# Performance work log

Hardware: AMD Instinct MI355X
Metric: run time of the kernel (lower is better)

## Reference

```python
import jax, jax.numpy as jnp
import numpy as np

N_STEPS = 3000
DT = 0.02


def make_phi_t(n=N_STEPS, dt=DT):
    # Central-difference first-derivative operator with one-sided 2nd-order ends.
    P = np.zeros((n, n), dtype=np.float32)
    P[0, 0:3] = [-1.5, 2.0, -0.5]
    idx = np.arange(1, n - 1)
    P[idx, idx - 1] = -0.5
    P[idx, idx + 1] = 0.5
    P[n - 1, n - 3:] = [0.5, -2.0, 1.5]
    return jnp.asarray(P / dt)


def lstm_layer(x, w_ih, w_hh, b_ih, b_hh):
    # x: [B, T, I]; PyTorch gate order i, f, g, o along the 4H axis.
    B, T, _ = x.shape
    H = w_hh.shape[1]
    x_proj = jnp.einsum('bti,gi->btg', x, w_ih) + b_ih + b_hh  # [B, T, 4H]

    def step(carry, xt):
        h, c = carry
        gates = xt + h @ w_hh.T  # [B, 4H]
        i, f, g, o = jnp.split(gates, 4, axis=-1)
        c = jax.nn.sigmoid(f) * c + jax.nn.sigmoid(i) * jnp.tanh(g)
        h = jax.nn.sigmoid(o) * jnp.tanh(c)
        return (h, c), h

    h0 = jnp.zeros((B, H), x.dtype)
    (_, _), hs = jax.lax.scan(step, (h0, h0), x_proj.transpose(1, 0, 2))
    return hs.transpose(1, 0, 2)  # [B, T, H]


def setup_inputs() -> dict:
    key = jax.random.key(0)
    B, T, I, H = 64, N_STEPS, 8, 128
    ks = jax.random.split(key, 16)
    s = lambda k, shape, fan: (jax.random.normal(k, shape, jnp.float32) / np.sqrt(fan)).astype(jnp.float32)
    return {
        'x': jax.random.normal(ks[0], (B, T, I), jnp.float32),
        'w_ih0': s(ks[1], (4 * H, I), I), 'w_hh0': s(ks[2], (4 * H, H), H),
        'b_ih0': s(ks[3], (4 * H,), H), 'b_hh0': s(ks[4], (4 * H,), H),
        'w_ih1': s(ks[5], (4 * H, H), H), 'w_hh1': s(ks[6], (4 * H, H), H),
        'b_ih1': s(ks[7], (4 * H,), H), 'b_hh1': s(ks[8], (4 * H,), H),
        'fc1_w': s(ks[9], (16, H), H), 'fc1_b': s(ks[10], (16,), H),
        'fc2_w': s(ks[11], (4, 16), 16), 'fc2_b': s(ks[12], (4,), 16),
        'fc3_w': s(ks[13], (1, 4), 4), 'fc3_b': s(ks[14], (1,), 4),
    }


def reference(x, w_ih0, w_hh0, b_ih0, b_hh0, w_ih1, w_hh1, b_ih1, b_hh1,
              fc1_w, fc1_b, fc2_w, fc2_b, fc3_w, fc3_b):
    phi = make_phi_t()  # fixed [3000, 3000] FD operator (buffer, not learned)
    h = lstm_layer(x, w_ih0, w_hh0, b_ih0, b_hh0)
    h = lstm_layer(h, w_ih1, w_hh1, b_ih1, b_hh1)
    h = jax.nn.relu(h @ fc1_w.T + fc1_b)
    h = jax.nn.relu(h @ fc2_w.T + fc2_b)
    y = h @ fc3_w.T + fc3_b            # [B, T, 1]
    yt = y[:, :, 0].T                  # [T, B]
    x_tt = phi @ (phi @ yt)            # double derivative via dense matmuls
    return x_tt.T[:, :, None]          # [B, T, 1]
```

## Files before the change

### kernel.cpp

```cpp
#include <hip/hip_runtime.h>
#include <math.h>


#define T_STEPS 3000
#define BATCH   64
#define HID     128
#define GATES   512
#define CHUNK   24
#define INV_DT  50.0f

__device__ __forceinline__ float sigmoid_(float x) {
    return 1.0f / (1.0f + __expf(-x));
}
__device__ __forceinline__ float tanh_(float x) {
    return 1.0f - 2.0f / (__expf(2.0f * x) + 1.0f);
}

__global__ __launch_bounds__(512, 2)
void lstm_layer0(const float* __restrict__ x,
                 const float* __restrict__ w_ih,
                 const float* __restrict__ w_hh,
                 const float* __restrict__ b_ih,
                 const float* __restrict__ b_hh,
                 float* __restrict__ h_out)
{
    const int b = blockIdx.x;
    const int g = threadIdx.x;
    const int j = g & (HID - 1);

    __shared__ __align__(16) float h_s[HID];
    __shared__ float part_f[HID], part_g[HID], part_o[HID];

    float w[HID];
#pragma unroll
    for (int i = 0; i < HID; i += 4) {
        float4 v = *(const float4*)(w_hh + (size_t)g * HID + i);
        w[i] = v.x; w[i+1] = v.y; w[i+2] = v.z; w[i+3] = v.w;
    }
    float wi[8];
#pragma unroll
    for (int i = 0; i < 8; i += 4) {
        float4 v = *(const float4*)(w_ih + (size_t)g * 8 + i);
        wi[i] = v.x; wi[i+1] = v.y; wi[i+2] = v.z; wi[i+3] = v.w;
    }
    const float bias = b_ih[g] + b_hh[g];
    float c = 0.0f;

    if (g < HID) h_s[g] = 0.0f;
    __syncthreads();

    const float* xrow = x + (size_t)b * T_STEPS * 8;
    float* hb = h_out + (size_t)b * T_STEPS * HID;

    for (int t = 0; t < T_STEPS; ++t) {
        float4 xa = *(const float4*)(xrow + t * 8);
        float4 xc = *(const float4*)(xrow + t * 8 + 4);
        float acc = bias
                  + wi[0]*xa.x + wi[1]*xa.y + wi[2]*xa.z + wi[3]*xa.w
                  + wi[4]*xc.x + wi[5]*xc.y + wi[6]*xc.z + wi[7]*xc.w;
#pragma unroll
        for (int k4 = 0; k4 < HID / 4; ++k4) {
            float4 h4 = *(const float4*)(&h_s[4 * k4]);
            acc += w[4*k4]*h4.x + w[4*k4+1]*h4.y + w[4*k4+2]*h4.z + w[4*k4+3]*h4.w;
        }

        float sig_i = 0.0f;
        if      (g < 128) sig_i    = sigmoid_(acc);
        else if (g < 256) part_f[j] = sigmoid_(acc);
        else if (g < 384) part_g[j] = tanh_(acc);
        else              part_o[j] = sigmoid_(acc);
        __syncthreads();

        if (g < 128) {
            c = part_f[j] * c + sig_i * part_g[j];
            float h = part_o[j] * tanh_(c);
            h_s[j] = h;
            hb[(size_t)t * HID + j] = h;
        }
        __syncthreads();
    }
}

__global__ __launch_bounds__(512, 2)
void lstm_layer1(const float* __restrict__ w_ih,
                 const float* __restrict__ w_hh,
                 const float* __restrict__ b_ih,
                 const float* __restrict__ b_hh,
                 float* __restrict__ h_buf)
{
    const int b = blockIdx.x;
    const int g = threadIdx.x;
    const int j = g & (HID - 1);

    __shared__ __align__(16) float xp[CHUNK][GATES];
    __shared__ __align__(16) float h_s[HID];
    __shared__ float part_f[HID], part_g[HID], part_o[HID];

    const float bias = b_ih[g] + b_hh[g];
    float c = 0.0f;
    if (g < HID) h_s[g] = 0.0f;

    float* hb = h_buf + (size_t)b * T_STEPS * HID;
    float w[HID];
    __syncthreads();

    for (int t0 = 0; t0 < T_STEPS; t0 += CHUNK) {
#pragma unroll
        for (int i = 0; i < HID; i += 4) {
            float4 v = *(const float4*)(w_ih + (size_t)g * HID + i);
            w[i] = v.x; w[i+1] = v.y; w[i+2] = v.z; w[i+3] = v.w;
        }
        for (int tg = 0; tg < CHUNK; tg += 8) {
            float a[8];
#pragma unroll
            for (int i = 0; i < 8; ++i) a[i] = bias;
            const float* hp = hb + (size_t)(t0 + tg) * HID;
#pragma unroll
            for (int k4 = 0; k4 < HID / 4; ++k4) {
#pragma unroll
                for (int i = 0; i < 8; ++i) {
                    float4 h4 = *(const float4*)(hp + i * HID + 4 * k4);
                    a[i] += w[4*k4]*h4.x + w[4*k4+1]*h4.y
                          + w[4*k4+2]*h4.z + w[4*k4+3]*h4.w;
                }
            }
#pragma unroll
            for (int i = 0; i < 8; ++i) xp[tg + i][g] = a[i];
        }
#pragma unroll
        for (int i = 0; i < HID; i += 4) {
            float4 v = *(const float4*)(w_hh + (size_t)g * HID + i);
            w[i] = v.x; w[i+1] = v.y; w[i+2] = v.z; w[i+3] = v.w;
        }
        __syncthreads();

        for (int tt = 0; tt < CHUNK; ++tt) {
            float acc = xp[tt][g];
#pragma unroll
            for (int k4 = 0; k4 < HID / 4; ++k4) {
                float4 h4 = *(const float4*)(&h_s[4 * k4]);
                acc += w[4*k4]*h4.x + w[4*k4+1]*h4.y + w[4*k4+2]*h4.z + w[4*k4+3]*h4.w;
            }
            float sig_i = 0.0f;
            if      (g < 128) sig_i    = sigmoid_(acc);
            else if (g < 256) part_f[j] = sigmoid_(acc);
            else if (g < 384) part_g[j] = tanh_(acc);
            else              part_o[j] = sigmoid_(acc);
            __syncthreads();
            if (g < 128) {
                c = part_f[j] * c + sig_i * part_g[j];
                float h = part_o[j] * tanh_(c);
                h_s[j] = h;
                hb[(size_t)(t0 + tt) * HID + j] = h;
            }
            __syncthreads();
        }
    }
}

__global__ void fc_head(const float* __restrict__ h_buf,
                        const float* __restrict__ fc1_w, const float* __restrict__ fc1_b,
                        const float* __restrict__ fc2_w, const float* __restrict__ fc2_b,
                        const float* __restrict__ fc3_w, const float* __restrict__ fc3_b,
                        float* __restrict__ y_t)
{
    int idx = blockIdx.x * blockDim.x + threadIdx.x;
    if (idx >= T_STEPS * BATCH) return;
    int t = idx >> 6, b = idx & 63;

    const float* h = h_buf + (size_t)b * T_STEPS * HID + (size_t)t * HID;
    float hv[HID];
#pragma unroll
    for (int k = 0; k < HID; k += 4) {
        float4 v = *(const float4*)(h + k);
        hv[k] = v.x; hv[k+1] = v.y; hv[k+2] = v.z; hv[k+3] = v.w;
    }
    float y1[16];
#pragma unroll
    for (int jo = 0; jo < 16; ++jo) {
        float a = fc1_b[jo];
#pragma unroll
        for (int k = 0; k < HID; k += 4) {
            float4 wv = *(const float4*)(fc1_w + jo * HID + k);
            a += wv.x*hv[k] + wv.y*hv[k+1] + wv.z*hv[k+2] + wv.w*hv[k+3];
        }
        y1[jo] = fmaxf(a, 0.0f);
    }
    float y2[4];
#pragma unroll
    for (int jo = 0; jo < 4; ++jo) {
        float a = fc2_b[jo];
#pragma unroll
        for (int k = 0; k < 16; ++k) a += fc2_w[jo * 16 + k] * y1[k];
        y2[jo] = fmaxf(a, 0.0f);
    }
    float y = fc3_b[0];
#pragma unroll
    for (int k = 0; k < 4; ++k) y += fc3_w[k] * y2[k];

    y_t[idx] = y;
}

__global__ void deriv_k(const float* __restrict__ in,
                        float* __restrict__ outp,
                        int transpose_out)
{
    int idx = blockIdx.x * blockDim.x + threadIdx.x;
    if (idx >= T_STEPS * BATCH) return;
    int t = idx >> 6, b = idx & 63;
    float v;
    if (t == 0) {
        v = (-1.5f * in[b] + 2.0f * in[64 + b] - 0.5f * in[128 + b]) * INV_DT;
    } else if (t == T_STEPS - 1) {
        v = (0.5f * in[(t-2)*64 + b] - 2.0f * in[(t-1)*64 + b] + 1.5f * in[t*64 + b]) * INV_DT;
    } else {
        v = (in[(t+1)*64 + b] - in[(t-1)*64 + b]) * (0.5f * INV_DT);
    }
    if (transpose_out) outp[(size_t)b * T_STEPS + t] = v;
    else               outp[idx] = v;
}

extern "C" void kernel_launch(void* const* d_in, const int* in_sizes, int n_in,
                              void* d_out, int out_size, void* d_ws, size_t ws_size,
                              hipStream_t stream)
{
    const float* x     = (const float*)d_in[0];
    const float* w_ih0 = (const float*)d_in[1];
    const float* w_hh0 = (const float*)d_in[2];
    const float* b_ih0 = (const float*)d_in[3];
    const float* b_hh0 = (const float*)d_in[4];
    const float* w_ih1 = (const float*)d_in[5];
    const float* w_hh1 = (const float*)d_in[6];
    const float* b_ih1 = (const float*)d_in[7];
    const float* b_hh1 = (const float*)d_in[8];
    const float* fc1_w = (const float*)d_in[9];
    const float* fc1_b = (const float*)d_in[10];
    const float* fc2_w = (const float*)d_in[11];
    const float* fc2_b = (const float*)d_in[12];
    const float* fc3_w = (const float*)d_in[13];
    const float* fc3_b = (const float*)d_in[14];
    float* out = (float*)d_out;

    float* h_buf = (float*)d_ws;
    float* y_t   = (float*)((char*)d_ws + 98304000);
    float* z_t   = (float*)((char*)d_ws + 98304000 + 768000);

    lstm_layer0<<<dim3(BATCH), dim3(512), 0, stream>>>(x, w_ih0, w_hh0, b_ih0, b_hh0, h_buf);
    lstm_layer1<<<dim3(BATCH), dim3(512), 0, stream>>>(w_ih1, w_hh1, b_ih1, b_hh1, h_buf);

    const int nelem = T_STEPS * BATCH;
    fc_head<<<dim3((nelem + 255) / 256), dim3(256), 0, stream>>>(
        h_buf, fc1_w, fc1_b, fc2_w, fc2_b, fc3_w, fc3_b, y_t);
    deriv_k<<<dim3((nelem + 255) / 256), dim3(256), 0, stream>>>(y_t, z_t, 0);
    deriv_k<<<dim3((nelem + 255) / 256), dim3(256), 0, stream>>>(z_t, out, 1);
}
```

Measured before the change: 16.63 ms.

## Interleave gate rows per lane and exchange gates via shuffles with one barrier

Thread mapping changes so the four gates for one hidden unit sit in adjacent lanes, which then exchange i/f/g/o activations with cross-lane shuffles instead of through shared memory. This removes one of the two block barriers per timestep by double-buffering h in shared memory. The dot products also use four independent accumulators to shorten the FMA dependency chain. The layer-1 input projection is restructured per timestep, and the occupancy hint moves to amdgpu_waves_per_eu.

Result: slower. 36.47 ms (+119.2%).

```diff
diff --git a/kernel.cpp b/kernel.cpp
--- a/kernel.cpp
+++ b/kernel.cpp
@@ -16,7 +16,8 @@
     return 1.0f - 2.0f / (__expf(2.0f * x) + 1.0f);
 }
 
-__global__ __launch_bounds__(512, 2)
+__global__ __launch_bounds__(512)
+__attribute__((amdgpu_waves_per_eu(2, 2)))
 void lstm_layer0(const float* __restrict__ x,
                  const float* __restrict__ w_ih,
                  const float* __restrict__ w_hh,
@@ -24,134 +25,153 @@
                  const float* __restrict__ b_hh,
                  float* __restrict__ h_out)
 {
-    const int b = blockIdx.x;
-    const int g = threadIdx.x;
-    const int j = g & (HID - 1);
-
-    __shared__ __align__(16) float h_s[HID];
-    __shared__ float part_f[HID], part_g[HID], part_o[HID];
+    const int b   = blockIdx.x;
+    const int tid = threadIdx.x;
+    const int j   = tid >> 2;
+    const int gt  = tid & 3;
+    const int r   = gt * HID + j;
+
+    __shared__ __align__(16) float h_s[2][HID];
 
     float w[HID];
 #pragma unroll
     for (int i = 0; i < HID; i += 4) {
-        float4 v = *(const float4*)(w_hh + (size_t)g * HID + i);
+        float4 v = *(const float4*)(w_hh + (size_t)r * HID + i);
         w[i] = v.x; w[i+1] = v.y; w[i+2] = v.z; w[i+3] = v.w;
     }
     float wi[8];
 #pragma unroll
     for (int i = 0; i < 8; i += 4) {
-        float4 v = *(const float4*)(w_ih + (size_t)g * 8 + i);
+        float4 v = *(const float4*)(w_ih + (size_t)r * 8 + i);
         wi[i] = v.x; wi[i+1] = v.y; wi[i+2] = v.z; wi[i+3] = v.w;
     }
-    const float bias = b_ih[g] + b_hh[g];
+    const float bias = b_ih[r] + b_hh[r];
     float c = 0.0f;
 
-    if (g < HID) h_s[g] = 0.0f;
+    if (tid < HID) h_s[0][tid] = 0.0f;
     __syncthreads();
 
     const float* xrow = x + (size_t)b * T_STEPS * 8;
     float* hb = h_out + (size_t)b * T_STEPS * HID;
 
     for (int t = 0; t < T_STEPS; ++t) {
+        const int rb = t & 1;
         float4 xa = *(const float4*)(xrow + t * 8);
         float4 xc = *(const float4*)(xrow + t * 8 + 4);
-        float acc = bias
-                  + wi[0]*xa.x + wi[1]*xa.y + wi[2]*xa.z + wi[3]*xa.w
-                  + wi[4]*xc.x + wi[5]*xc.y + wi[6]*xc.z + wi[7]*xc.w;
-#pragma unroll
-        for (int k4 = 0; k4 < HID / 4; ++k4) {
-            float4 h4 = *(const float4*)(&h_s[4 * k4]);
-            acc += w[4*k4]*h4.x + w[4*k4+1]*h4.y + w[4*k4+2]*h4.z + w[4*k4+3]*h4.w;
-        }
-
-        float sig_i = 0.0f;
-        if      (g < 128) sig_i    = sigmoid_(acc);
-        else if (g < 256) part_f[j] = sigmoid_(acc);
-        else if (g < 384) part_g[j] = tanh_(acc);
-        else              part_o[j] = sigmoid_(acc);
+        float acc0 = bias
+                   + wi[0]*xa.x + wi[1]*xa.y + wi[2]*xa.z + wi[3]*xa.w
+                   + wi[4]*xc.x + wi[5]*xc.y + wi[6]*xc.z + wi[7]*xc.w;
+        float acc1 = 0.0f, acc2 = 0.0f, acc3 = 0.0f;
+#pragma unroll
+        for (int k4 = 0; k4 < HID / 4; k4 += 4) {
+            float4 h0 = *(const float4*)(&h_s[rb][4*k4]);
+            float4 h1 = *(const float4*)(&h_s[rb][4*k4 + 4]);
+            float4 h2 = *(const float4*)(&h_s[rb][4*k4 + 8]);
+            float4 h3 = *(const float4*)(&h_s[rb][4*k4 + 12]);
+            acc0 += w[4*k4   ]*h0.x + w[4*k4+ 1]*h0.y + w[4*k4+ 2]*h0.z + w[4*k4+ 3]*h0.w;
+            acc1 += w[4*k4+ 4]*h1.x + w[4*k4+ 5]*h1.y + w[4*k4+ 6]*h1.z + w[4*k4+ 7]*h1.w;
+            acc2 += w[4*k4+ 8]*h2.x + w[4*k4+ 9]*h2.y + w[4*k4+10]*h2.z + w[4*k4+11]*h2.w;
+            acc3 += w[4*k4+12]*h3.x + w[4*k4+13]*h3.y + w[4*k4+14]*h3.z + w[4*k4+15]*h3.w;
+        }
+        float accs = (acc0 + acc1) + (acc2 + acc3);
+
+        float av = (gt == 2) ? tanh_(accs) : sigmoid_(accs);
+        float t1 = __shfl_xor(av, 1);
+        float t2 = __shfl_xor(av, 2);
+        float t3 = __shfl_xor(t1, 2);
+        if (gt == 0) {
+            c = t1 * c + av * t2;
+            float h = t3 * tanh_(c);
+            h_s[rb ^ 1][j] = h;
+            hb[(size_t)t * HID + j] = h;
+        }
         __syncthreads();
-
-        if (g < 128) {
-            c = part_f[j] * c + sig_i * part_g[j];
-            float h = part_o[j] * tanh_(c);
-            h_s[j] = h;
-            hb[(size_t)t * HID + j] = h;
-        }
-        __syncthreads();
-    }
-}
-
-__global__ __launch_bounds__(512, 2)
+    }
+}
+
+__global__ __launch_bounds__(512)
+__attribute__((amdgpu_waves_per_eu(2, 2)))
 void lstm_layer1(const float* __restrict__ w_ih,
                  const float* __restrict__ w_hh,
                  const float* __restrict__ b_ih,
                  const float* __restrict__ b_hh,
                  float* __restrict__ h_buf)
 {
-    const int b = blockIdx.x;
-    const int g = threadIdx.x;
-    const int j = g & (HID - 1);
-
-    __shared__ __align__(16) float xp[CHUNK][GATES];
-    __shared__ __align__(16) float h_s[HID];
-    __shared__ float part_f[HID], part_g[HID], part_o[HID];
-
-    const float bias = b_ih[g] + b_hh[g];
+    const int b   = blockIdx.x;
+    const int tid = threadIdx.x;
+    const int j   = tid >> 2;
+    const int gt  = tid & 3;
+    const int r   = gt * HID + j;
+
+    __shared__ __align__(16) float xp_s[CHUNK][GATES];
+    __shared__ __align__(16) float h_s[2][HID];
+
+    const float bias = b_ih[r] + b_hh[r];
     float c = 0.0f;
-    if (g < HID) h_s[g] = 0.0f;
-
-    float* hb = h_buf + (size_t)b * T_STEPS * HID;
+    if (tid < HID) h_s[0][tid] = 0.0f;
+    __syncthreads();
+
+    float* hbB = h_buf + (size_t)b * T_STEPS * HID;
     float w[HID];
-    __syncthreads();
 
     for (int t0 = 0; t0 < T_STEPS; t0 += CHUNK) {
 #pragma unroll
         for (int i = 0; i < HID; i += 4) {
-            float4 v = *(const float4*)(w_ih + (size_t)g * HID + i);
+            float4 v = *(const float4*)(w_ih + (size_t)r * HID + i);
             w[i] = v.x; w[i+1] = v.y; w[i+2] = v.z; w[i+3] = v.w;
         }
-        for (int tg = 0; tg < CHUNK; tg += 8) {
-            float a[8];
-#pragma unroll
-            for (int i = 0; i < 8; ++i) a[i] = bias;
-            const float* hp = hb + (size_t)(t0 + tg) * HID;
-#pragma unroll
-            for (int k4 = 0; k4 < HID / 4; ++k4) {
-#pragma unroll
-                for (int i = 0; i < 8; ++i) {
-                    float4 h4 = *(const float4*)(hp + i * HID + 4 * k4);
-                    a[i] += w[4*k4]*h4.x + w[4*k4+1]*h4.y
-                          + w[4*k4+2]*h4.z + w[4*k4+3]*h4.w;
-                }
+        const float* hp = hbB + (size_t)t0 * HID;
+#pragma unroll 2
+        for (int tau = 0; tau < CHUNK; ++tau) {
+            float a0 = bias, a1 = 0.0f, a2 = 0.0f, a3 = 0.0f;
+#pragma unroll
+            for (int k4 = 0; k4 < HID / 4; k4 += 4) {
+                float4 h0 = *(const float4*)(hp + tau*HID + 4*k4);
+                float4 h1 = *(const float4*)(hp + tau*HID + 4*k4 + 4);
+                float4 h2 = *(const float4*)(hp + tau*HID + 4*k4 + 8);
+                float4 h3 = *(const float4*)(hp + tau*HID + 4*k4 + 12);
+                a0 += w[4*k4   ]*h0.x + w[4*k4+ 1]*h0.y + w[4*k4+ 2]*h0.z + w[4*k4+ 3]*h0.w;
+                a1 += w[4*k4+ 4]*h1.x + w[4*k4+ 5]*h1.y + w[4*k4+ 6]*h1.z + w[4*k4+ 7]*h1.w;
+                a2 += w[4*k4+ 8]*h2.x + w[4*k4+ 9]*h2.y + w[4*k4+10]*h2.z + w[4*k4+11]*h2.w;
+                a3 += w[4*k4+12]*h3.x + w[4*k4+13]*h3.y + w[4*k4+14]*h3.z + w[4*k4+15]*h3.w;
             }
-#pragma unroll
-            for (int i = 0; i < 8; ++i) xp[tg + i][g] = a[i];
+            xp_s[tau][tid] = (a0 + a1) + (a2 + a3);
         }
 #pragma unroll
         for (int i = 0; i < HID; i += 4) {
-            float4 v = *(const float4*)(w_hh + (size_t)g * HID + i);
+            float4 v = *(const float4*)(w_hh + (size_t)r * HID + i);
             w[i] = v.x; w[i+1] = v.y; w[i+2] = v.z; w[i+3] = v.w;
         }
         __syncthreads();
 
+#pragma unroll 1
         for (int tt = 0; tt < CHUNK; ++tt) {
-            float acc = xp[tt][g];
-#pragma unroll
-            for (int k4 = 0; k4 < HID / 4; ++k4) {
-                float4 h4 = *(const float4*)(&h_s[4 * k4]);
-                acc += w[4*k4]*h4.x + w[4*k4+1]*h4.y + w[4*k4+2]*h4.z + w[4*k4+3]*h4.w;
+            const int t  = t0 + tt;
+            const int rb = t & 1;
+            float acc0 = xp_s[tt][tid];
+            float acc1 = 0.0f, acc2 = 0.0f, acc3 = 0.0f;
+#pragma unroll
+            for (int k4 = 0; k4 < HID / 4; k4 += 4) {
+                float4 h0 = *(const float4*)(&h_s[rb][4*k4]);
+                float4 h1 = *(const float4*)(&h_s[rb][4*k4 + 4]);
+                float4 h2 = *(const float4*)(&h_s[rb][4*k4 + 8]);
+                float4 h3 = *(const float4*)(&h_s[rb][4*k4 + 12]);
+                acc0 += w[4*k4   ]*h0.x + w[4*k4+ 1]*h0.y + w[4*k4+ 2]*h0.z + w[4*k4+ 3]*h0.w;
+                acc1 += w[4*k4+ 4]*h1.x + w[4*k4+ 5]*h1.y + w[4*k4+ 6]*h1.z + w[4*k4+ 7]*h1.w;
+                acc2 += w[4*k4+ 8]*h2.x + w[4*k4+ 9]*h2.y + w[4*k4+10]*h2.z + w[4*k4+11]*h2.w;
+                acc3 += w[4*k4+12]*h3.x + w[4*k4+13]*h3.y + w[4*k4+14]*h3.z + w[4*k4+15]*h3.w;
             }
-            float sig_i = 0.0f;
-            if      (g < 128) sig_i    = sigmoid_(acc);
-            else if (g < 256) part_f[j] = sigmoid_(acc);
-            else if (g < 384) part_g[j] = tanh_(acc);
-            else              part_o[j] = sigmoid_(acc);
-            __syncthreads();
-            if (g < 128) {
-                c = part_f[j] * c + sig_i * part_g[j];
-                float h = part_o[j] * tanh_(c);
-                h_s[j] = h;
-                hb[(size_t)(t0 + tt) * HID + j] = h;
+            float accs = (acc0 + acc1) + (acc2 + acc3);
+
+            float av = (gt == 2) ? tanh_(accs) : sigmoid_(accs);
+            float t1 = __shfl_xor(av, 1);
+            float t2 = __shfl_xor(av, 2);
+            float t3 = __shfl_xor(t1, 2);
+            if (gt == 0) {
+                c = t1 * c + av * t2;
+                float h = t3 * tanh_(c);
+                h_s[rb ^ 1][j] = h;
+                hbB[(size_t)t * HID + j] = h;
             }
             __syncthreads();
         }
```
